# Kernel optimization log

Measured on AMD Instinct MI355X. Metric: run time of the kernel, lower is better.

The kernel has to match this reference:

```python
import jax, jax.numpy as jnp
import numpy as np

N_NODES = 50000
N_EDGES = 400000
D_IN = 512
DIM_H = 256
N_GRAPHS = 64
BN_EPS = 1e-5


def _linear_init(key, din, dout):
    kw, kb = jax.random.split(key)
    s = 1.0 / np.sqrt(din)
    W = jax.random.uniform(kw, (din, dout), jnp.float32, -s, s)
    b = jax.random.uniform(kb, (dout,), jnp.float32, -s, s)
    return W, b


def setup_inputs() -> dict:
    key = jax.random.key(0)
    ks = iter(jax.random.split(key, 64))
    inp = {}
    inp["x"] = jax.random.normal(next(ks), (N_NODES, D_IN), jnp.float32)
    inp["edge_index"] = jax.random.randint(next(ks), (2, N_EDGES), 0, N_NODES, jnp.int32)
    inp["batch"] = jnp.sort(jax.random.randint(next(ks), (N_NODES,), 0, N_GRAPHS, jnp.int32))
    dins = [D_IN, DIM_H, DIM_H]
    for l in range(3):
        p = "c%d_" % (l + 1)
        inp[p + "W1"], inp[p + "b1"] = _linear_init(next(ks), dins[l], DIM_H)
        inp[p + "gamma"] = jax.random.uniform(next(ks), (DIM_H,), jnp.float32, 0.5, 1.5)
        inp[p + "beta"] = 0.1 * jax.random.normal(next(ks), (DIM_H,), jnp.float32)
        inp[p + "mean"] = 0.1 * jax.random.normal(next(ks), (DIM_H,), jnp.float32)
        inp[p + "var"] = jax.random.uniform(next(ks), (DIM_H,), jnp.float32, 0.5, 1.5)
        inp[p + "W2"], inp[p + "b2"] = _linear_init(next(ks), DIM_H, DIM_H)
    inp["lin1_W"], inp["lin1_b"] = _linear_init(next(ks), 3 * DIM_H, 64)
    inp["lin2_W"], inp["lin2_b"] = _linear_init(next(ks), 64, 2)
    return inp


def _gin_layer(x, src, dst, W1, b1, gamma, beta, mean, var, W2, b2):
    # GINConv with eps=0: h_i = MLP(x_i + sum_{j->i} x_j); scatter-add over edges
    agg = jax.ops.segment_sum(x[src], dst, num_segments=x.shape[0])
    h = (x + agg) @ W1 + b1
    # eval-mode BatchNorm1d
    h = jax.nn.relu((h - mean) * jax.lax.rsqrt(var + BN_EPS) * gamma + beta)
    return jax.nn.relu(h @ W2 + b2)


def reference(x, edge_index, batch,
              c1_W1, c1_b1, c1_gamma, c1_beta, c1_mean, c1_var, c1_W2, c1_b2,
              c2_W1, c2_b1, c2_gamma, c2_beta, c2_mean, c2_var, c2_W2, c2_b2,
              c3_W1, c3_b1, c3_gamma, c3_beta, c3_mean, c3_var, c3_W2, c3_b2,
              lin1_W, lin1_b, lin2_W, lin2_b):
    src, dst = edge_index[0], edge_index[1]
    h1 = _gin_layer(x, src, dst, c1_W1, c1_b1, c1_gamma, c1_beta, c1_mean, c1_var, c1_W2, c1_b2)
    h2 = _gin_layer(h1, src, dst, c2_W1, c2_b1, c2_gamma, c2_beta, c2_mean, c2_var, c2_W2, c2_b2)
    h3 = _gin_layer(h2, src, dst, c3_W1, c3_b1, c3_gamma, c3_beta, c3_mean, c3_var, c3_W2, c3_b2)
    # global_add_pool per graph
    p1 = jax.ops.segment_sum(h1, batch, num_segments=N_GRAPHS)
    p2 = jax.ops.segment_sum(h2, batch, num_segments=N_GRAPHS)
    p3 = jax.ops.segment_sum(h3, batch, num_segments=N_GRAPHS)
    h = jnp.concatenate([p1, p2, p3], axis=1)
    h = jax.nn.relu(h @ lin1_W + lin1_b)
    # Dropout(p=0.8) is identity in eval mode
    h = h @ lin2_W + lin2_b
    return (h, jax.nn.log_softmax(h, axis=1))
```

## Files before the change

### kernel.cpp

```cpp
#include <hip/hip_runtime.h>
#include <hip/hip_bf16.h>

#define DIV_UP(a,b) (((a)+(b)-1)/(b))

static const int NN  = 50000;
static const int NE  = 400000;
static const int DIN = 512;
static const int DH  = 256;
static const int NG  = 64;
static const int MAXDEG = 64;

typedef unsigned short u16;
typedef unsigned int   u32;
typedef __attribute__((ext_vector_type(8))) short bf16x8;
typedef __attribute__((ext_vector_type(4))) float f32x4;

#define AS1(p) ((const __attribute__((address_space(1))) void*)(p))
#define AS3(p) ((__attribute__((address_space(3))) void*)(p))

__device__ inline u16 f2bf(float f) {
  u32 u = __float_as_uint(f);
  u += 0x7fffu + ((u >> 16) & 1u);
  return (u16)(u >> 16);
}
__device__ inline float bf2f(u16 h) { return __uint_as_float(((u32)h) << 16); }
__device__ inline void unpack2(u32 u, float& lo, float& hi) {
  lo = __uint_as_float(u << 16);
  hi = __uint_as_float(u & 0xffff0000u);
}
__device__ inline u32 pack2(float lo, float hi) {
  return (u32)f2bf(lo) | ((u32)f2bf(hi) << 16);
}

struct SetupArgs {
  const float* x; u16* Xb;
  const float* Wsrc[6]; u16* Wdst[6];
  const float* bn[15];
  float* scsh;
  int* cnt; float* PL;
};
static const int NB_X = (NN * DIN / 8) / 256;
static const int NB_W = (131072 + 5 * 65536) / 256;
static const int NB_Z = DIV_UP(NN + NG * 768, 256);

__global__ __launch_bounds__(256) void k_setup(SetupArgs a) {
  int b = blockIdx.x;
  if (b < NB_X) {
    int i = b * 256 + threadIdx.x;
    const float4* p = (const float4*)a.x + (size_t)i * 2;
    float4 f0 = p[0], f1 = p[1];
    uint4 o;
    o.x = pack2(f0.x, f0.y); o.y = pack2(f0.z, f0.w);
    o.z = pack2(f1.x, f1.y); o.w = pack2(f1.z, f1.w);
    ((uint4*)a.Xb)[i] = o;
  } else if (b < NB_X + NB_W) {
    int idx = (b - NB_X) * 256 + threadIdx.x;
    if (idx < 131072) {
      int n = idx >> 9, k = idx & 511;
      a.Wdst[0][idx] = f2bf(a.Wsrc[0][(size_t)k * 256 + n]);
    } else {
      int r = idx - 131072;
      int s = 1 + (r >> 16);
      int ri = r & 65535;
      int n = ri >> 8, k = ri & 255;
      a.Wdst[s][ri] = f2bf(a.Wsrc[s][(size_t)k * 256 + n]);
    }
  } else if (b < NB_X + NB_W + 3) {
    int l = b - NB_X - NB_W, ch = threadIdx.x;
    float sc = rsqrtf(a.bn[l * 5 + 4][ch] + 1e-5f) * a.bn[l * 5 + 1][ch];
    float sh = (a.bn[l * 5 + 0][ch] - a.bn[l * 5 + 3][ch]) * sc + a.bn[l * 5 + 2][ch];
    a.scsh[l * 512 + ch] = sc;
    a.scsh[l * 512 + 256 + ch] = sh;
  } else {
    int i = (b - NB_X - NB_W - 3) * 256 + threadIdx.x;
    if (i < NN) a.cnt[i] = 0;
    else if (i - NN < NG * 768) a.PL[i - NN] = 0.f;
  }
}

__global__ __launch_bounds__(256) void k_fill2(const int* __restrict__ src,
                                               const int* __restrict__ dst,
                                               int* __restrict__ cnt,
                                               int* __restrict__ adj, int nE) {
  int e = blockIdx.x * 256 + threadIdx.x;
  if (e >= nE) return;
  int d = dst[e];
  int pos = atomicAdd(&cnt[d], 1);
  if (pos < MAXDEG) adj[(size_t)d * MAXDEG + pos] = src[e];
}

__global__ __launch_bounds__(256) void k_gather_bn(const u16* __restrict__ Y,
                                                   const int* __restrict__ cnt,
                                                   const int* __restrict__ adj,
                                                   const float* __restrict__ scsh,
                                                   u16* __restrict__ A) {
  int gid = blockIdx.x * 256 + threadIdx.x;
  int i = gid >> 5;
  if (i >= NN) return;
  int c = (gid & 31) << 3;
  uint4 v = *(const uint4*)(Y + (size_t)i * DH + c);
  float a0,a1,a2,a3,a4,a5,a6,a7;
  unpack2(v.x,a0,a1); unpack2(v.y,a2,a3); unpack2(v.z,a4,a5); unpack2(v.w,a6,a7);
  int deg = cnt[i]; if (deg > MAXDEG) deg = MAXDEG;
  const int* row = adj + (size_t)i * MAXDEG;
  int e = 0;
  for (; e + 8 <= deg; e += 8) {
    uint4 w[8];
#pragma unroll
    for (int u = 0; u < 8; ++u)
      w[u] = *(const uint4*)(Y + (size_t)row[e + u] * DH + c);
#pragma unroll
    for (int u = 0; u < 8; ++u) {
      float b0,b1,b2,b3,b4,b5,b6,b7;
      unpack2(w[u].x,b0,b1); unpack2(w[u].y,b2,b3);
      unpack2(w[u].z,b4,b5); unpack2(w[u].w,b6,b7);
      a0+=b0; a1+=b1; a2+=b2; a3+=b3; a4+=b4; a5+=b5; a6+=b6; a7+=b7;
    }
  }
  for (; e + 4 <= deg; e += 4) {
    uint4 w[4];
#pragma unroll
    for (int u = 0; u < 4; ++u)
      w[u] = *(const uint4*)(Y + (size_t)row[e + u] * DH + c);
#pragma unroll
    for (int u = 0; u < 4; ++u) {
      float b0,b1,b2,b3,b4,b5,b6,b7;
      unpack2(w[u].x,b0,b1); unpack2(w[u].y,b2,b3);
      unpack2(w[u].z,b4,b5); unpack2(w[u].w,b6,b7);
      a0+=b0; a1+=b1; a2+=b2; a3+=b3; a4+=b4; a5+=b5; a6+=b6; a7+=b7;
    }
  }
  for (; e < deg; ++e) {
    uint4 w = *(const uint4*)(Y + (size_t)row[e] * DH + c);
    float b0,b1,b2,b3,b4,b5,b6,b7;
    unpack2(w.x,b0,b1); unpack2(w.y,b2,b3); unpack2(w.z,b4,b5); unpack2(w.w,b6,b7);
    a0+=b0; a1+=b1; a2+=b2; a3+=b3; a4+=b4; a5+=b5; a6+=b6; a7+=b7;
  }
  float4 sc0 = *(const float4*)(scsh + c);
  float4 sc1 = *(const float4*)(scsh + c + 4);
  float4 sh0 = *(const float4*)(scsh + 256 + c);
  float4 sh1 = *(const float4*)(scsh + 256 + c + 4);
  a0 = fmaxf(fmaf(a0, sc0.x, sh0.x), 0.f);
  a1 = fmaxf(fmaf(a1, sc0.y, sh0.y), 0.f);
  a2 = fmaxf(fmaf(a2, sc0.z, sh0.z), 0.f);
  a3 = fmaxf(fmaf(a3, sc0.w, sh0.w), 0.f);
  a4 = fmaxf(fmaf(a4, sc1.x, sh1.x), 0.f);
  a5 = fmaxf(fmaf(a5, sc1.y, sh1.y), 0.f);
  a6 = fmaxf(fmaf(a6, sc1.z, sh1.z), 0.f);
  a7 = fmaxf(fmaf(a7, sc1.w, sh1.w), 0.f);
  uint4 o;
  o.x = pack2(a0,a1); o.y = pack2(a2,a3); o.z = pack2(a4,a5); o.w = pack2(a6,a7);
  *(uint4*)(A + (size_t)i * DH + c) = o;
}

template <int MODE, int POOL, int STORE, int K>
__global__ __launch_bounds__(512, 4) void k_gemm_mfma(
    const u16* __restrict__ A, const u16* __restrict__ BT,
    const float* __restrict__ bias, u16* __restrict__ out,
    const int* __restrict__ batch, float* __restrict__ PL, int poolOff, int M) {
  const int N = 256;
  __shared__ __align__(16) u16 sm[32768];
  __shared__ int bsh[128];
  u16* Cs = sm;
  const int bm = blockIdx.x * 128;
  const int tid = threadIdx.x;
  const int lane = tid & 63;
  const int wave = tid >> 6;
  const int wm = (wave >> 2) * 64;
  const int wn = (wave & 3) * 64;
  const int l15 = lane & 15;
  const int l4 = lane >> 4;
  const int srow = lane >> 2;
  const int scol = (lane & 3) * 8;

  if (POOL && tid < 128) {
    int gm = bm + tid;
    bsh[tid] = (gm < M) ? batch[gm] : -1;
  }

  auto STAGE = [&](int buf, int k0) {
    u16* As = sm + buf * 12288;
    u16* Bs = As + 4096;
    {
      int row = wave * 16 + srow;
      int grA = bm + row; if (grA >= M) grA = M - 1;
      __builtin_amdgcn_global_load_lds(AS1(A + (size_t)grA * K + k0 + scol),
                                       AS3(As + wave * 512), 16, 0, 0);
    }
#pragma unroll
    for (int i = 0; i < 2; ++i) {
      int q = wave * 2 + i;
      int row = q * 16 + srow;
      __builtin_amdgcn_global_load_lds(AS1(BT + (size_t)row * K + k0 + scol),
                                       AS3(Bs + q * 512), 16, 0, 0);
    }
  };

  f32x4 acc[4][4] = {};
  const int nt = K >> 5;
  STAGE(0, 0);
  int cur = 0;
  for (int t = 0; t < nt; ++t) {
    __syncthreads();
    if (t + 1 < nt) STAGE(cur ^ 1, (t + 1) << 5);
    u16* As = sm + cur * 12288;
    u16* Bs = As + 4096;
    bf16x8 af[4], bf_[4];
#pragma unroll
    for (int f = 0; f < 4; ++f) {
      af[f]  = *(const bf16x8*)(As + (wm + f * 16 + l15) * 32 + l4 * 8);
      bf_[f] = *(const bf16x8*)(Bs + (wn + f * 16 + l15) * 32 + l4 * 8);
    }
#pragma unroll
    for (int i = 0; i < 4; ++i)
#pragma unroll
      for (int j = 0; j < 4; ++j)
        acc[i][j] = __builtin_amdgcn_mfma_f32_16x16x32_bf16(af[i], bf_[j], acc[i][j], 0, 0, 0);
    cur ^= 1;
  }

  __syncthreads();
#pragma unroll
  for (int j = 0; j < 4; ++j) {
    int n = wn + j * 16 + l15;
    float sh = (MODE == 1) ? bias[n] : 0.f;
#pragma unroll
    for (int i = 0; i < 4; ++i) {
#pragma unroll
      for (int r = 0; r < 4; ++r) {
        int row = wm + i * 16 + l4 * 4 + r;
        float v = acc[i][j][r] + sh;
        if (MODE == 1) v = fmaxf(v, 0.f);
        Cs[row * 256 + n] = f2bf(v);
      }
    }
  }
  __syncthreads();

  if (STORE) {
    const int ccol = (tid & 31) * 8;
#pragma unroll
    for (int p = 0; p < 8; ++p) {
      int row = p * 16 + (tid >> 5);
      int gm = bm + row;
      if (gm < M)
        *(uint4*)(out + (size_t)gm * N + ccol) =
            *(const uint4*)(Cs + row * 256 + ccol);
    }
  }

  if (POOL) {
    int col = tid & 255;
    int half = tid >> 8;
    float accv = 0.f;
    int cg = bsh[half * 64];
    for (int r = 0; r < 64; ++r) {
      int row = half * 64 + r;
      int g = bsh[row];
      if (g != cg) {
        if (cg >= 0) unsafeAtomicAdd(&PL[cg * 768 + poolOff + col], accv);
        accv = 0.f;
        cg = g;
      }
      accv += bf2f(Cs[row * 256 + col]);
    }
    if (cg >= 0) unsafeAtomicAdd(&PL[cg * 768 + poolOff + col], accv);
  }
}

__global__ __launch_bounds__(64) void k_head1(const float* __restrict__ P,
                                              const float* __restrict__ W,
                                              const float* __restrict__ b,
                                              float* __restrict__ Q) {
  __shared__ float pr[768];
  int g = blockIdx.x, t = threadIdx.x;
  for (int i = t; i < 768; i += 64) pr[i] = P[g * 768 + i];
  __syncthreads();
  float acc = b[t];
  for (int k = 0; k < 768; ++k) acc = fmaf(pr[k], W[k * 64 + t], acc);
  Q[g * 64 + t] = fmaxf(acc, 0.f);
}

__global__ __launch_bounds__(64) void k_head2(const float* __restrict__ Q,
                                              const float* __restrict__ W,
                                              const float* __restrict__ b,
                                              float* __restrict__ out) {
  int g = threadIdx.x;
  if (g >= 64) return;
  float h0 = b[0], h1 = b[1];
  for (int k = 0; k < 64; ++k) {
    float q = Q[g * 64 + k];
    h0 = fmaf(q, W[k * 2 + 0], h0);
    h1 = fmaf(q, W[k * 2 + 1], h1);
  }
  out[g * 2 + 0] = h0;
  out[g * 2 + 1] = h1;
  float m = fmaxf(h0, h1);
  float lse = m + logf(expf(h0 - m) + expf(h1 - m));
  out[128 + g * 2 + 0] = h0 - lse;
  out[128 + g * 2 + 1] = h1 - lse;
}

extern "C" void kernel_launch(void* const* d_in, const int* in_sizes, int n_in,
                              void* d_out, int out_size, void* d_ws,
                              size_t ws_size, hipStream_t stream) {
  const float* x = (const float*)d_in[0];
  const int* ei = (const int*)d_in[1];
  const int* batch = (const int*)d_in[2];
  const float* W1[3]; const float* b1[3]; const float* ga[3]; const float* be[3];
  const float* mu[3]; const float* va[3]; const float* W2[3]; const float* b2[3];
  for (int l = 0; l < 3; ++l) {
    int base = 3 + 8 * l;
    W1[l] = (const float*)d_in[base + 0];
    b1[l] = (const float*)d_in[base + 1];
    ga[l] = (const float*)d_in[base + 2];
    be[l] = (const float*)d_in[base + 3];
    mu[l] = (const float*)d_in[base + 4];
    va[l] = (const float*)d_in[base + 5];
    W2[l] = (const float*)d_in[base + 6];
    b2[l] = (const float*)d_in[base + 7];
  }
  const float* l1W = (const float*)d_in[27];
  const float* l1b = (const float*)d_in[28];
  const float* l2W = (const float*)d_in[29];
  const float* l2b = (const float*)d_in[30];
  const int* src = ei;
  const int* dst = ei + NE;
  float* out = (float*)d_out;

  char* w = (char*)d_ws;
  u16* Xb  = (u16*)w; w += (size_t)NN * DIN * 2;
  u16* Yb  = (u16*)w; w += (size_t)NN * DH * 2;
  u16* Ab  = (u16*)w; w += (size_t)NN * DH * 2;
  u16* H1b = (u16*)w; w += (size_t)NN * DH * 2;
  u16* H2b = (u16*)w; w += (size_t)NN * DH * 2;
  u16* W1T[3]; u16* W2T[3];
  W1T[0] = (u16*)w; w += (size_t)DIN * DH * 2;
  for (int l = 1; l < 3; ++l) { W1T[l] = (u16*)w; w += (size_t)DH * DH * 2; }
  for (int l = 0; l < 3; ++l) { W2T[l] = (u16*)w; w += (size_t)DH * DH * 2; }
  float* scsh = (float*)w; w += 3 * 512 * 4;
  float* PL = (float*)w; w += NG * 768 * 4;
  float* Q  = (float*)w; w += NG * 64 * 4;
  int* cnt  = (int*)w; w += (size_t)NN * 4;
  int* adj  = (int*)w; w += (size_t)NN * MAXDEG * 4;

  SetupArgs sa;
  sa.x = x; sa.Xb = Xb;
  sa.Wsrc[0] = W1[0]; sa.Wdst[0] = W1T[0];
  sa.Wsrc[1] = W1[1]; sa.Wdst[1] = W1T[1];
  sa.Wsrc[2] = W1[2]; sa.Wdst[2] = W1T[2];
  for (int l = 0; l < 3; ++l) { sa.Wsrc[3 + l] = W2[l]; sa.Wdst[3 + l] = W2T[l]; }
  for (int l = 0; l < 3; ++l) {
    sa.bn[l * 5 + 0] = b1[l]; sa.bn[l * 5 + 1] = ga[l]; sa.bn[l * 5 + 2] = be[l];
    sa.bn[l * 5 + 3] = mu[l]; sa.bn[l * 5 + 4] = va[l];
  }
  sa.scsh = scsh; sa.cnt = cnt; sa.PL = PL;
  k_setup<<<NB_X + NB_W + 3 + NB_Z, 256, 0, stream>>>(sa);

  k_fill2<<<DIV_UP(NE, 256), 256, 0, stream>>>(src, dst, cnt, adj, NE);

  const int gg = DIV_UP(NN, 128);
  const u16* hin[3] = {Xb, H1b, H2b};
  u16* hout[3] = {H1b, H2b, H1b};

  for (int l = 0; l < 3; ++l) {
    if (l == 0)
      k_gemm_mfma<2, 0, 1, 512><<<gg, 512, 0, stream>>>(hin[l], W1T[l], nullptr, Yb,
                                                        nullptr, nullptr, 0, NN);
    else
      k_gemm_mfma<2, 0, 1, 256><<<gg, 512, 0, stream>>>(hin[l], W1T[l], nullptr, Yb,
                                                        nullptr, nullptr, 0, NN);
    k_gather_bn<<<DIV_UP(NN * 32, 256), 256, 0, stream>>>(Yb, cnt, adj,
                                                          scsh + l * 512, Ab);
    if (l < 2)
      k_gemm_mfma<1, 1, 1, 256><<<gg, 512, 0, stream>>>(Ab, W2T[l], b2[l], hout[l],
                                                        batch, PL, 256 * l, NN);
    else
      k_gemm_mfma<1, 1, 0, 256><<<gg, 512, 0, stream>>>(Ab, W2T[l], b2[l], hout[l],
                                                        batch, PL, 256 * l, NN);
  }

  k_head1<<<NG, 64, 0, stream>>>(PL, l1W, l1b, Q);
  k_head2<<<1, 64, 0, stream>>>(Q, l2W, l2b, out);
}
```

Measured before the change: 287.9 us.

## Fuse neighbor gather and BN into second GEMM with swizzled LDS layout

```diff
diff --git a/kernel.cpp b/kernel.cpp
--- a/kernel.cpp
+++ b/kernel.cpp
@@ -89,20 +89,14 @@
   if (pos < MAXDEG) adj[(size_t)d * MAXDEG + pos] = src[e];
 }
 
-__global__ __launch_bounds__(256) void k_gather_bn(const u16* __restrict__ Y,
-                                                   const int* __restrict__ cnt,
-                                                   const int* __restrict__ adj,
-                                                   const float* __restrict__ scsh,
-                                                   u16* __restrict__ A) {
-  int gid = blockIdx.x * 256 + threadIdx.x;
-  int i = gid >> 5;
-  if (i >= NN) return;
-  int c = (gid & 31) << 3;
-  uint4 v = *(const uint4*)(Y + (size_t)i * DH + c);
-  float a0,a1,a2,a3,a4,a5,a6,a7;
+__device__ inline void gather_row(const u16* __restrict__ Y, const int* __restrict__ cnt,
+                                  const int* __restrict__ adj, int gr, int c,
+                                  float& a0, float& a1, float& a2, float& a3,
+                                  float& a4, float& a5, float& a6, float& a7) {
+  uint4 v = *(const uint4*)(Y + (size_t)gr * DH + c);
   unpack2(v.x,a0,a1); unpack2(v.y,a2,a3); unpack2(v.z,a4,a5); unpack2(v.w,a6,a7);
-  int deg = cnt[i]; if (deg > MAXDEG) deg = MAXDEG;
-  const int* row = adj + (size_t)i * MAXDEG;
+  int deg = cnt[gr]; if (deg > MAXDEG) deg = MAXDEG;
+  const int* row = adj + (size_t)gr * MAXDEG;
   int e = 0;
   for (; e + 8 <= deg; e += 8) {
     uint4 w[8];
@@ -136,31 +130,14 @@
     unpack2(w.x,b0,b1); unpack2(w.y,b2,b3); unpack2(w.z,b4,b5); unpack2(w.w,b6,b7);
     a0+=b0; a1+=b1; a2+=b2; a3+=b3; a4+=b4; a5+=b5; a6+=b6; a7+=b7;
   }
-  float4 sc0 = *(const float4*)(scsh + c);
-  float4 sc1 = *(const float4*)(scsh + c + 4);
-  float4 sh0 = *(const float4*)(scsh + 256 + c);
-  float4 sh1 = *(const float4*)(scsh + 256 + c + 4);
-  a0 = fmaxf(fmaf(a0, sc0.x, sh0.x), 0.f);
-  a1 = fmaxf(fmaf(a1, sc0.y, sh0.y), 0.f);
-  a2 = fmaxf(fmaf(a2, sc0.z, sh0.z), 0.f);
-  a3 = fmaxf(fmaf(a3, sc0.w, sh0.w), 0.f);
-  a4 = fmaxf(fmaf(a4, sc1.x, sh1.x), 0.f);
-  a5 = fmaxf(fmaf(a5, sc1.y, sh1.y), 0.f);
-  a6 = fmaxf(fmaf(a6, sc1.z, sh1.z), 0.f);
-  a7 = fmaxf(fmaf(a7, sc1.w, sh1.w), 0.f);
-  uint4 o;
-  o.x = pack2(a0,a1); o.y = pack2(a2,a3); o.z = pack2(a4,a5); o.w = pack2(a6,a7);
-  *(uint4*)(A + (size_t)i * DH + c) = o;
-}
-
-template <int MODE, int POOL, int STORE, int K>
-__global__ __launch_bounds__(512, 4) void k_gemm_mfma(
+}
+
+template <int K>
+__global__ __launch_bounds__(512, 4) void k_gemm1(
     const u16* __restrict__ A, const u16* __restrict__ BT,
-    const float* __restrict__ bias, u16* __restrict__ out,
-    const int* __restrict__ batch, float* __restrict__ PL, int poolOff, int M) {
+    u16* __restrict__ out, int M) {
   const int N = 256;
   __shared__ __align__(16) u16 sm[32768];
-  __shared__ int bsh[128];
   u16* Cs = sm;
   const int bm = blockIdx.x * 128;
   const int tid = threadIdx.x;
@@ -170,13 +147,9 @@
   const int wn = (wave & 3) * 64;
   const int l15 = lane & 15;
   const int l4 = lane >> 4;
+  const int sw = (lane >> 1) & 3;
   const int srow = lane >> 2;
-  const int scol = (lane & 3) * 8;
-
-  if (POOL && tid < 128) {
-    int gm = bm + tid;
-    bsh[tid] = (gm < M) ? batch[gm] : -1;
-  }
+  const int sslot = (lane & 3) ^ ((lane >> 3) & 3);
 
   auto STAGE = [&](int buf, int k0) {
     u16* As = sm + buf * 12288;
@@ -184,14 +157,14 @@
     {
       int row = wave * 16 + srow;
       int grA = bm + row; if (grA >= M) grA = M - 1;
-      __builtin_amdgcn_global_load_lds(AS1(A + (size_t)grA * K + k0 + scol),
+      __builtin_amdgcn_global_load_lds(AS1(A + (size_t)grA * K + k0 + sslot * 8),
                                        AS3(As + wave * 512), 16, 0, 0);
     }
 #pragma unroll
     for (int i = 0; i < 2; ++i) {
       int q = wave * 2 + i;
       int row = q * 16 + srow;
-      __builtin_amdgcn_global_load_lds(AS1(BT + (size_t)row * K + k0 + scol),
+      __builtin_amdgcn_global_load_lds(AS1(BT + (size_t)row * K + k0 + sslot * 8),
                                        AS3(Bs + q * 512), 16, 0, 0);
     }
   };
@@ -208,8 +181,8 @@
     bf16x8 af[4], bf_[4];
 #pragma unroll
     for (int f = 0; f < 4; ++f) {
-      af[f]  = *(const bf16x8*)(As + (wm + f * 16 + l15) * 32 + l4 * 8);
-      bf_[f] = *(const bf16x8*)(Bs + (wn + f * 16 + l15) * 32 + l4 * 8);
+      af[f]  = *(const bf16x8*)(As + (wm + f * 16 + l15) * 32 + ((l4 ^ sw) << 3));
+      bf_[f] = *(const bf16x8*)(Bs + (wn + f * 16 + l15) * 32 + ((l4 ^ sw) << 3));
     }
 #pragma unroll
     for (int i = 0; i < 4; ++i)
@@ -223,15 +196,125 @@
 #pragma unroll
   for (int j = 0; j < 4; ++j) {
     int n = wn + j * 16 + l15;
-    float sh = (MODE == 1) ? bias[n] : 0.f;
 #pragma unroll
     for (int i = 0; i < 4; ++i) {
 #pragma unroll
       for (int r = 0; r < 4; ++r) {
         int row = wm + i * 16 + l4 * 4 + r;
-        float v = acc[i][j][r] + sh;
-        if (MODE == 1) v = fmaxf(v, 0.f);
-        Cs[row * 256 + n] = f2bf(v);
+        Cs[row * 256 + n] = f2bf(acc[i][j][r]);
+      }
+    }
+  }
+  __syncthreads();
+  const int ccol = (tid & 31) * 8;
+#pragma unroll
+  for (int p = 0; p < 8; ++p) {
+    int row = p * 16 + (tid >> 5);
+    int gm = bm + row;
+    if (gm < M)
+      *(uint4*)(out + (size_t)gm * N + ccol) = *(const uint4*)(Cs + row * 256 + ccol);
+  }
+}
+
+template <int STORE>
+__global__ __launch_bounds__(512, 4) void k_gin2(
+    const u16* __restrict__ Y, const int* __restrict__ cnt,
+    const int* __restrict__ adj, const float* __restrict__ scsh,
+    const u16* __restrict__ BT, const float* __restrict__ bias,
+    u16* __restrict__ out, const int* __restrict__ batch,
+    float* __restrict__ PL, int poolOff, int M) {
+  __shared__ __align__(16) u16 At[64 * 256];
+  __shared__ __align__(16) u16 Bs[2][8192];
+  __shared__ int bsh[64];
+  const int bm = blockIdx.x * 64;
+  const int tid = threadIdx.x;
+  const int lane = tid & 63;
+  const int wave = tid >> 6;
+  const int wm = (wave >> 2) * 32;
+  const int wn = (wave & 3) * 64;
+  const int l15 = lane & 15;
+  const int l4 = lane >> 4;
+  const int sw = (lane >> 1) & 3;
+  const int a7 = lane & 7;
+  const int sslot = (lane & 3) ^ ((lane >> 3) & 3);
+
+  if (tid < 64) bsh[tid] = (bm + tid < M) ? batch[bm + tid] : -1;
+
+  auto STAGE_B = [&](int buf, int k0) {
+#pragma unroll
+    for (int i = 0; i < 2; ++i) {
+      int q = wave * 2 + i;
+      int row = q * 16 + (lane >> 2);
+      __builtin_amdgcn_global_load_lds(AS1(BT + (size_t)row * 256 + k0 + sslot * 8),
+                                       AS3(&Bs[buf][q * 512]), 16, 0, 0);
+    }
+  };
+
+  STAGE_B(0, 0);
+
+  {
+    const int c = (tid & 31) << 3;
+    float4 sc0 = *(const float4*)(scsh + c);
+    float4 sc1 = *(const float4*)(scsh + c + 4);
+    float4 sh0 = *(const float4*)(scsh + 256 + c);
+    float4 sh1 = *(const float4*)(scsh + 256 + c + 4);
+    const int slot0 = c >> 3;
+#pragma unroll 1
+    for (int p = 0; p < 4; ++p) {
+      int rl = p * 16 + (tid >> 5);
+      int gr = bm + rl; if (gr >= M) gr = M - 1;
+      float a0,a1,a2,a3,a4,a5,a6,a7v;
+      gather_row(Y, cnt, adj, gr, c, a0,a1,a2,a3,a4,a5,a6,a7v);
+      a0 = fmaxf(fmaf(a0, sc0.x, sh0.x), 0.f);
+      a1 = fmaxf(fmaf(a1, sc0.y, sh0.y), 0.f);
+      a2 = fmaxf(fmaf(a2, sc0.z, sh0.z), 0.f);
+      a3 = fmaxf(fmaf(a3, sc0.w, sh0.w), 0.f);
+      a4 = fmaxf(fmaf(a4, sc1.x, sh1.x), 0.f);
+      a5 = fmaxf(fmaf(a5, sc1.y, sh1.y), 0.f);
+      a6 = fmaxf(fmaf(a6, sc1.z, sh1.z), 0.f);
+      a7v = fmaxf(fmaf(a7v, sc1.w, sh1.w), 0.f);
+      uint4 o;
+      o.x = pack2(a0,a1); o.y = pack2(a2,a3); o.z = pack2(a4,a5); o.w = pack2(a6,a7v);
+      *(uint4*)(At + rl * 256 + ((slot0 ^ (rl & 7)) << 3)) = o;
+    }
+  }
+
+  f32x4 acc[2][4] = {};
+  int cur = 0;
+  for (int t = 0; t < 8; ++t) {
+    __syncthreads();
+    if (t + 1 < 8) STAGE_B(cur ^ 1, (t + 1) << 5);
+    bf16x8 af[2], bf_[4];
+#pragma unroll
+    for (int f = 0; f < 2; ++f) {
+      int row = wm + f * 16 + l15;
+      af[f] = *(const bf16x8*)(At + row * 256 + ((((t << 2) + l4) ^ a7) << 3));
+    }
+#pragma unroll
+    for (int j = 0; j < 4; ++j) {
+      int row = wn + j * 16 + l15;
+      bf_[j] = *(const bf16x8*)(&Bs[cur][row * 32 + ((l4 ^ sw) << 3)]);
+    }
+#pragma unroll
+    for (int i = 0; i < 2; ++i)
+#pragma unroll
+      for (int j = 0; j < 4; ++j)
+        acc[i][j] = __builtin_amdgcn_mfma_f32_16x16x32_bf16(af[i], bf_[j], acc[i][j], 0, 0, 0);
+    cur ^= 1;
+  }
+
+  __syncthreads();
+  u16* Cs = At;
+#pragma unroll
+  for (int j = 0; j < 4; ++j) {
+    int n = wn + j * 16 + l15;
+    float sh = bias[n];
+#pragma unroll
+    for (int i = 0; i < 2; ++i) {
+#pragma unroll
+      for (int r = 0; r < 4; ++r) {
+        int row = wm + i * 16 + l4 * 4 + r;
+        Cs[row * 256 + n] = f2bf(fmaxf(acc[i][j][r] + sh, 0.f));
       }
     }
   }
@@ -240,22 +323,21 @@
   if (STORE) {
     const int ccol = (tid & 31) * 8;
 #pragma unroll
-    for (int p = 0; p < 8; ++p) {
+    for (int p = 0; p < 4; ++p) {
       int row = p * 16 + (tid >> 5);
       int gm = bm + row;
       if (gm < M)
-        *(uint4*)(out + (size_t)gm * N + ccol) =
-            *(const uint4*)(Cs + row * 256 + ccol);
-    }
-  }
-
-  if (POOL) {
+        *(uint4*)(out + (size_t)gm * DH + ccol) = *(const uint4*)(Cs + row * 256 + ccol);
+    }
+  }
+
+  {
     int col = tid & 255;
     int half = tid >> 8;
     float accv = 0.f;
-    int cg = bsh[half * 64];
-    for (int r = 0; r < 64; ++r) {
-      int row = half * 64 + r;
+    int cg = bsh[half * 32];
+    for (int r = 0; r < 32; ++r) {
+      int row = half * 32 + r;
       int g = bsh[row];
       if (g != cg) {
         if (cg >= 0) unsafeAtomicAdd(&PL[cg * 768 + poolOff + col], accv);
@@ -331,7 +413,6 @@
   char* w = (char*)d_ws;
   u16* Xb  = (u16*)w; w += (size_t)NN * DIN * 2;
   u16* Yb  = (u16*)w; w += (size_t)NN * DH * 2;
-  u16* Ab  = (u16*)w; w += (size_t)NN * DH * 2;
   u16* H1b = (u16*)w; w += (size_t)NN * DH * 2;
   u16* H2b = (u16*)w; w += (size_t)NN * DH * 2;
   u16* W1T[3]; u16* W2T[3];
@@ -359,25 +440,22 @@
 
   k_fill2<<<DIV_UP(NE, 256), 256, 0, stream>>>(src, dst, cnt, adj, NE);
 
-  const int gg = DIV_UP(NN, 128);
+  const int g1 = DIV_UP(NN, 128);
+  const int g2 = DIV_UP(NN, 64);
   const u16* hin[3] = {Xb, H1b, H2b};
   u16* hout[3] = {H1b, H2b, H1b};
 
   for (int l = 0; l < 3; ++l) {
     if (l == 0)
-      k_gemm_mfma<2, 0, 1, 512><<<gg, 512, 0, stream>>>(hin[l], W1T[l], nullptr, Yb,
-                                                        nullptr, nullptr, 0, NN);
+      k_gemm1<512><<<g1, 512, 0, stream>>>(hin[l], W1T[l], Yb, NN);
     else
-      k_gemm_mfma<2, 0, 1, 256><<<gg, 512, 0, stream>>>(hin[l], W1T[l], nullptr, Yb,
-                                                        nullptr, nullptr, 0, NN);
-    k_gather_bn<<<DIV_UP(NN * 32, 256), 256, 0, stream>>>(Yb, cnt, adj,
-                                                          scsh + l * 512, Ab);
+      k_gemm1<256><<<g1, 512, 0, stream>>>(hin[l], W1T[l], Yb, NN);
     if (l < 2)
-      k_gemm_mfma<1, 1, 1, 256><<<gg, 512, 0, stream>>>(Ab, W2T[l], b2[l], hout[l],
-                                                        batch, PL, 256 * l, NN);
+      k_gin2<1><<<g2, 512, 0, stream>>>(Yb, cnt, adj, scsh + l * 512, W2T[l],
+                                        b2[l], hout[l], batch, PL, 256 * l, NN);
     else
-      k_gemm_mfma<1, 1, 0, 256><<<gg, 512, 0, stream>>>(Ab, W2T[l], b2[l], hout[l],
-                                                        batch, PL, 256 * l, NN);
+      k_gin2<0><<<g2, 512, 0, stream>>>(Yb, cnt, adj, scsh + l * 512, W2T[l],
+                                        b2[l], hout[l], batch, PL, 256 * l, NN);
   }
 
   k_head1<<<NG, 64, 0, stream>>>(PL, l1W, l1b, Q);
```

After: 278.9 us. 1.03x faster.

## Fuse fp32-to-bf16 input conversion into first GEMM and swizzle LDS tiles

Applied to the files above, without the earlier changes.

```diff
diff --git a/kernel.cpp b/kernel.cpp
--- a/kernel.cpp
+++ b/kernel.cpp
@@ -33,28 +33,18 @@
 }
 
 struct SetupArgs {
-  const float* x; u16* Xb;
   const float* Wsrc[6]; u16* Wdst[6];
   const float* bn[15];
   float* scsh;
   int* cnt; float* PL;
 };
-static const int NB_X = (NN * DIN / 8) / 256;
 static const int NB_W = (131072 + 5 * 65536) / 256;
 static const int NB_Z = DIV_UP(NN + NG * 768, 256);
 
 __global__ __launch_bounds__(256) void k_setup(SetupArgs a) {
   int b = blockIdx.x;
-  if (b < NB_X) {
-    int i = b * 256 + threadIdx.x;
-    const float4* p = (const float4*)a.x + (size_t)i * 2;
-    float4 f0 = p[0], f1 = p[1];
-    uint4 o;
-    o.x = pack2(f0.x, f0.y); o.y = pack2(f0.z, f0.w);
-    o.z = pack2(f1.x, f1.y); o.w = pack2(f1.z, f1.w);
-    ((uint4*)a.Xb)[i] = o;
-  } else if (b < NB_X + NB_W) {
-    int idx = (b - NB_X) * 256 + threadIdx.x;
+  if (b < NB_W) {
+    int idx = b * 256 + threadIdx.x;
     if (idx < 131072) {
       int n = idx >> 9, k = idx & 511;
       a.Wdst[0][idx] = f2bf(a.Wsrc[0][(size_t)k * 256 + n]);
@@ -65,14 +55,14 @@
       int n = ri >> 8, k = ri & 255;
       a.Wdst[s][ri] = f2bf(a.Wsrc[s][(size_t)k * 256 + n]);
     }
-  } else if (b < NB_X + NB_W + 3) {
-    int l = b - NB_X - NB_W, ch = threadIdx.x;
+  } else if (b < NB_W + 3) {
+    int l = b - NB_W, ch = threadIdx.x;
     float sc = rsqrtf(a.bn[l * 5 + 4][ch] + 1e-5f) * a.bn[l * 5 + 1][ch];
     float sh = (a.bn[l * 5 + 0][ch] - a.bn[l * 5 + 3][ch]) * sc + a.bn[l * 5 + 2][ch];
     a.scsh[l * 512 + ch] = sc;
     a.scsh[l * 512 + 256 + ch] = sh;
   } else {
-    int i = (b - NB_X - NB_W - 3) * 256 + threadIdx.x;
+    int i = (b - NB_W - 3) * 256 + threadIdx.x;
     if (i < NN) a.cnt[i] = 0;
     else if (i - NN < NG * 768) a.PL[i - NN] = 0.f;
   }
@@ -153,11 +143,12 @@
   *(uint4*)(A + (size_t)i * DH + c) = o;
 }
 
-template <int MODE, int POOL, int STORE, int K>
-__global__ __launch_bounds__(512, 4) void k_gemm_mfma(
-    const u16* __restrict__ A, const u16* __restrict__ BT,
-    const float* __restrict__ bias, u16* __restrict__ out,
-    const int* __restrict__ batch, float* __restrict__ PL, int poolOff, int M) {
+template <int K, int F32A, int MODE, int POOL, int STORE>
+__global__ __launch_bounds__(512, 4) void k_gemm(
+    const u16* __restrict__ A, const float* __restrict__ A32,
+    const u16* __restrict__ BT, const float* __restrict__ bias,
+    u16* __restrict__ out, const int* __restrict__ batch,
+    float* __restrict__ PL, int poolOff, int M) {
   const int N = 256;
   __shared__ __align__(16) u16 sm[32768];
   __shared__ int bsh[128];
@@ -170,8 +161,9 @@
   const int wn = (wave & 3) * 64;
   const int l15 = lane & 15;
   const int l4 = lane >> 4;
+  const int sw = (lane >> 1) & 3;
   const int srow = lane >> 2;
-  const int scol = (lane & 3) * 8;
+  const int sslot = (lane & 3) ^ ((lane >> 3) & 3);
 
   if (POOL && tid < 128) {
     int gm = bm + tid;
@@ -184,14 +176,24 @@
     {
       int row = wave * 16 + srow;
       int grA = bm + row; if (grA >= M) grA = M - 1;
-      __builtin_amdgcn_global_load_lds(AS1(A + (size_t)grA * K + k0 + scol),
-                                       AS3(As + wave * 512), 16, 0, 0);
+      if (F32A) {
+        const float* s = A32 + (size_t)grA * K + k0 + sslot * 8;
+        float4 f0 = *(const float4*)s;
+        float4 f1 = *(const float4*)(s + 4);
+        uint4 o;
+        o.x = pack2(f0.x, f0.y); o.y = pack2(f0.z, f0.w);
+        o.z = pack2(f1.x, f1.y); o.w = pack2(f1.z, f1.w);
+        *(uint4*)(As + row * 32 + (lane & 3) * 8) = o;
+      } else {
+        __builtin_amdgcn_global_load_lds(AS1(A + (size_t)grA * K + k0 + sslot * 8),
+                                         AS3(As + wave * 512), 16, 0, 0);
+      }
     }
 #pragma unroll
     for (int i = 0; i < 2; ++i) {
       int q = wave * 2 + i;
       int row = q * 16 + srow;
-      __builtin_amdgcn_global_load_lds(AS1(BT + (size_t)row * K + k0 + scol),
+      __builtin_amdgcn_global_load_lds(AS1(BT + (size_t)row * K + k0 + sslot * 8),
                                        AS3(Bs + q * 512), 16, 0, 0);
     }
   };
@@ -208,8 +210,8 @@
     bf16x8 af[4], bf_[4];
 #pragma unroll
     for (int f = 0; f < 4; ++f) {
-      af[f]  = *(const bf16x8*)(As + (wm + f * 16 + l15) * 32 + l4 * 8);
-      bf_[f] = *(const bf16x8*)(Bs + (wn + f * 16 + l15) * 32 + l4 * 8);
+      af[f]  = *(const bf16x8*)(As + (wm + f * 16 + l15) * 32 + ((l4 ^ sw) << 3));
+      bf_[f] = *(const bf16x8*)(Bs + (wn + f * 16 + l15) * 32 + ((l4 ^ sw) << 3));
     }
 #pragma unroll
     for (int i = 0; i < 4; ++i)
@@ -244,8 +246,7 @@
       int row = p * 16 + (tid >> 5);
       int gm = bm + row;
       if (gm < M)
-        *(uint4*)(out + (size_t)gm * N + ccol) =
-            *(const uint4*)(Cs + row * 256 + ccol);
+        *(uint4*)(out + (size_t)gm * N + ccol) = *(const uint4*)(Cs + row * 256 + ccol);
     }
   }
 
@@ -329,7 +330,6 @@
   float* out = (float*)d_out;
 
   char* w = (char*)d_ws;
-  u16* Xb  = (u16*)w; w += (size_t)NN * DIN * 2;
   u16* Yb  = (u16*)w; w += (size_t)NN * DH * 2;
   u16* Ab  = (u16*)w; w += (size_t)NN * DH * 2;
   u16* H1b = (u16*)w; w += (size_t)NN * DH * 2;
@@ -345,7 +345,6 @@
   int* adj  = (int*)w; w += (size_t)NN * MAXDEG * 4;
 
   SetupArgs sa;
-  sa.x = x; sa.Xb = Xb;
   sa.Wsrc[0] = W1[0]; sa.Wdst[0] = W1T[0];
   sa.Wsrc[1] = W1[1]; sa.Wdst[1] = W1T[1];
   sa.Wsrc[2] = W1[2]; sa.Wdst[2] = W1T[2];
@@ -355,29 +354,29 @@
     sa.bn[l * 5 + 3] = mu[l]; sa.bn[l * 5 + 4] = va[l];
   }
   sa.scsh = scsh; sa.cnt = cnt; sa.PL = PL;
-  k_setup<<<NB_X + NB_W + 3 + NB_Z, 256, 0, stream>>>(sa);
+  k_setup<<<NB_W + 3 + NB_Z, 256, 0, stream>>>(sa);
 
   k_fill2<<<DIV_UP(NE, 256), 256, 0, stream>>>(src, dst, cnt, adj, NE);
 
-  const int gg = DIV_UP(NN, 128);
-  const u16* hin[3] = {Xb, H1b, H2b};
+  const int g1 = DIV_UP(NN, 128);
+  const int gg = DIV_UP(NN * 32, 256);
+  const u16* hin[3] = {nullptr, H1b, H2b};
   u16* hout[3] = {H1b, H2b, H1b};
 
   for (int l = 0; l < 3; ++l) {
     if (l == 0)
-      k_gemm_mfma<2, 0, 1, 512><<<gg, 512, 0, stream>>>(hin[l], W1T[l], nullptr, Yb,
-                                                        nullptr, nullptr, 0, NN);
+      k_gemm<512, 1, 0, 0, 1><<<g1, 512, 0, stream>>>(nullptr, x, W1T[0], nullptr,
+                                                      Yb, nullptr, nullptr, 0, NN);
     else
-      k_gemm_mfma<2, 0, 1, 256><<<gg, 512, 0, stream>>>(hin[l], W1T[l], nullptr, Yb,
-                                                        nullptr, nullptr, 0, NN);
-    k_gather_bn<<<DIV_UP(NN * 32, 256), 256, 0, stream>>>(Yb, cnt, adj,
-                                                          scsh + l * 512, Ab);
+      k_gemm<256, 0, 0, 0, 1><<<g1, 512, 0, stream>>>(hin[l], nullptr, W1T[l], nullptr,
+                                                      Yb, nullptr, nullptr, 0, NN);
+    k_gather_bn<<<gg, 256, 0, stream>>>(Yb, cnt, adj, scsh + l * 512, Ab);
     if (l < 2)
-      k_gemm_mfma<1, 1, 1, 256><<<gg, 512, 0, stream>>>(Ab, W2T[l], b2[l], hout[l],
-                                                        batch, PL, 256 * l, NN);
+      k_gemm<256, 0, 1, 1, 1><<<g1, 512, 0, stream>>>(Ab, nullptr, W2T[l], b2[l],
+                                                      hout[l], batch, PL, 256 * l, NN);
     else
-      k_gemm_mfma<1, 1, 0, 256><<<gg, 512, 0, stream>>>(Ab, W2T[l], b2[l], hout[l],
-                                                        batch, PL, 256 * l, NN);
+      k_gemm<256, 0, 1, 1, 0><<<g1, 512, 0, stream>>>(Ab, nullptr, W2T[l], b2[l],
+                                                      hout[l], batch, PL, 256 * l, NN);
   }
 
   k_head1<<<NG, 64, 0, stream>>>(PL, l1W, l1b, Q);
```

New measurement: 267.9 us. -7.0%, faster.
